# Kernel optimization log

Hardware: AMD Instinct MI355X
Metric: run time of the kernel (lower is better)

## Reference

```python
import jax, jax.numpy as jnp
import numpy as np

N, E, DIM, H = 100000, 1600000, 128, 8
HD = DIM // H


def setup_inputs() -> dict:
    key = jax.random.key(0)
    ks = jax.random.split(key, 12)
    inp = {
        'x': jax.random.normal(ks[0], (N, DIM), dtype=jnp.float32),
        'src': jax.random.randint(ks[1], (E,), 0, N, dtype=jnp.int32),
        'dst': jax.random.randint(ks[2], (E,), 0, N, dtype=jnp.int32),
    }
    scale = 1.0 / np.sqrt(DIM)
    for i, nm in enumerate(['q', 'k', 'v', 'o']):
        inp['W' + nm] = jax.random.normal(ks[3 + 2 * i], (DIM, DIM), dtype=jnp.float32) * scale
        inp['b' + nm] = jax.random.normal(ks[4 + 2 * i], (DIM,), dtype=jnp.float32) * 0.01
    return inp


def reference(x, src, dst, Wq, bq, Wk, bk, Wv, bv, Wo, bo):
    n = x.shape[0]
    q = (x @ Wq + bq).reshape(n, H, HD)
    k = (x @ Wk + bk).reshape(n, H, HD)
    v = (x @ Wv + bv).reshape(n, H, HD)
    # per-edge score: dot(q[src], k[dst]) over head_dim  -> [E, H]
    scores = jnp.einsum('ehd,ehd->eh', q[src], k[dst]) / np.sqrt(HD).astype(np.float32)
    # edge softmax grouped by destination node
    m = jax.ops.segment_max(scores, dst, num_segments=n)        # [N, H]
    e = jnp.exp(scores - m[dst])                                 # [E, H]
    z = jax.ops.segment_sum(e, dst, num_segments=n)              # [N, H]
    attn = e / z[dst]                                            # [E, H]
    # weighted scatter-sum of source values into destinations
    agg = jax.ops.segment_sum(v[src] * attn[:, :, None], dst, num_segments=n)  # [N, H, HD]
    out = agg.reshape(n, DIM) @ Wo + bo
    return out
```

## Files before the change

### kernel.cpp

```cpp
#include <hip/hip_runtime.h>
#include <hip/hip_bf16.h>
#include <math.h>


#define CAP 64
#define CUR_STRIDE 16
#define BCHUNK 4096

typedef __attribute__((ext_vector_type(8))) short short8;
typedef __attribute__((ext_vector_type(4))) float f32x4;

__device__ inline unsigned short f2bf(float f) {
    unsigned u = __float_as_uint(f);
    unsigned r = u + 0x7fffu + ((u >> 16) & 1u);
    return (unsigned short)(r >> 16);
}
__device__ inline float bfhi2f(unsigned u) { return __uint_as_float(u & 0xffff0000u); }
__device__ inline float bflo2f(unsigned u) { return __uint_as_float(u << 16); }

__device__ inline float w_perm(const float* Wq, const float* Wk, const float* Wv,
                               int k, int c) {
    if (c < 256) {
        int g = c >> 2, r = c & 3;
        return (r < 2) ? Wq[k * 128 + 2 * g + r] : Wv[k * 128 + 2 * g + (r - 2)];
    }
    return Wk[k * 128 + (c - 256)];
}

__global__ void pack_b_kernel(const float* __restrict__ Wq, const float* __restrict__ Wk,
                              const float* __restrict__ Wv, const float* __restrict__ Wo,
                              const float* __restrict__ bq, const float* __restrict__ bk,
                              const float* __restrict__ bv,
                              short* __restrict__ BqkvP, short* __restrict__ BoP,
                              float* __restrict__ bqkv) {
    int t = blockIdx.x * 256 + threadIdx.x;
    if (t < 24 * 4 * 64 * 8) {
        int j = t & 7, l = (t >> 3) & 63, ks = (t >> 9) & 3, ct = t >> 11;
        int c = ct * 16 + (l & 15);
        int k = ks * 32 + (l >> 4) * 8 + j;
        BqkvP[t] = (short)f2bf(w_perm(Wq, Wk, Wv, k, c));
    }
    if (t < 8 * 4 * 64 * 8) {
        int j = t & 7, l = (t >> 3) & 63, ks = (t >> 9) & 3, ct = t >> 11;
        int c = ct * 16 + (l & 15);
        int k = ks * 32 + (l >> 4) * 8 + j;
        BoP[t] = (short)f2bf(Wo[k * 128 + c]);
    }
    if (t < 384) {
        float v;
        if (t < 256) {
            int g = t >> 2, r = t & 3;
            v = (r < 2) ? bq[2 * g + r] : bv[2 * g + (r - 2)];
        } else v = bk[t - 256];
        bqkv[t] = v;
    }
}

#define QKV_STRIDE 392
__global__ __launch_bounds__(256) void gemm_qkv_mfma(const float* __restrict__ A,
        const short* __restrict__ Bp, const float* __restrict__ bias,
        short* __restrict__ qv, short* __restrict__ kb, int M) {
    __shared__ short stage[4][16][QKV_STRIDE];
    int w = threadIdx.x >> 6, l = threadIdx.x & 63;
    int row0 = blockIdx.x * 64 + w * 16;
    int lr = l & 15, lk = l >> 4;

    f32x4 acc[24];
    #pragma unroll
    for (int ct = 0; ct < 24; ++ct) {
        float b = bias[ct * 16 + lr];
        acc[ct][0] = b; acc[ct][1] = b; acc[ct][2] = b; acc[ct][3] = b;
    }

    int arow = row0 + lr;
    bool rowok = arow < M;
    const float* arp = A + (size_t)arow * 128;

    #pragma unroll
    for (int ks = 0; ks < 4; ++ks) {
        f32x4 a0 = {0.f, 0.f, 0.f, 0.f}, a1 = {0.f, 0.f, 0.f, 0.f};
        if (rowok) {
            a0 = *(const f32x4*)(arp + ks * 32 + lk * 8);
            a1 = *(const f32x4*)(arp + ks * 32 + lk * 8 + 4);
        }
        short8 af;
        af[0] = (short)f2bf(a0[0]); af[1] = (short)f2bf(a0[1]);
        af[2] = (short)f2bf(a0[2]); af[3] = (short)f2bf(a0[3]);
        af[4] = (short)f2bf(a1[0]); af[5] = (short)f2bf(a1[1]);
        af[6] = (short)f2bf(a1[2]); af[7] = (short)f2bf(a1[3]);
        #pragma unroll
        for (int ct = 0; ct < 24; ++ct) {
            short8 bf = *(const short8*)(Bp + ((size_t)(ct * 4 + ks) * 64 + l) * 8);
            acc[ct] = __builtin_amdgcn_mfma_f32_16x16x32_bf16(af, bf, acc[ct], 0, 0, 0);
        }
    }

    #pragma unroll
    for (int ct = 0; ct < 24; ++ct) {
        int c = ct * 16 + lr;
        #pragma unroll
        for (int j = 0; j < 4; ++j)
            stage[w][lk * 4 + j][c] = (short)f2bf(acc[ct][j]);
    }
    __syncthreads();

    #pragma unroll
    for (int it = 0; it < 8; ++it) {
        int rr = it * 2 + (l >> 5);
        int row = row0 + rr;
        if (row < M) {
            short8 vqv = *(const short8*)&stage[w][rr][(l & 31) * 8];
            *(short8*)(qv + (size_t)row * 256 + (l & 31) * 8) = vqv;
        }
    }
    #pragma unroll
    for (int it = 0; it < 4; ++it) {
        int rr = it * 4 + (l >> 4);
        int row = row0 + rr;
        if (row < M) {
            short8 vk = *(const short8*)&stage[w][rr][256 + (l & 15) * 8];
            *(short8*)(kb + (size_t)row * 128 + (l & 15) * 8) = vk;
        }
    }
}

__global__ __launch_bounds__(256) void gemm_out_mfma(const short* __restrict__ A,
        const short* __restrict__ Bp, const float* __restrict__ bias,
        float* __restrict__ C, int M) {
    int w = threadIdx.x >> 6, l = threadIdx.x & 63;
    int row0 = blockIdx.x * 64 + w * 16;
    int lr = l & 15, lk = l >> 4;

    f32x4 acc[8];
    #pragma unroll
    for (int ct = 0; ct < 8; ++ct) {
        float b = bias[ct * 16 + lr];
        acc[ct][0] = b; acc[ct][1] = b; acc[ct][2] = b; acc[ct][3] = b;
    }

    int arow = row0 + lr;
    bool rowok = arow < M;
    const short* arp = A + (size_t)arow * 128;

    #pragma unroll
    for (int ks = 0; ks < 4; ++ks) {
        short8 af = {0, 0, 0, 0, 0, 0, 0, 0};
        if (rowok) af = *(const short8*)(arp + ks * 32 + lk * 8);
        #pragma unroll
        for (int ct = 0; ct < 8; ++ct) {
            short8 bf = *(const short8*)(Bp + ((size_t)(ct * 4 + ks) * 64 + l) * 8);
            acc[ct] = __builtin_amdgcn_mfma_f32_16x16x32_bf16(af, bf, acc[ct], 0, 0, 0);
        }
    }

    #pragma unroll
    for (int ct = 0; ct < 8; ++ct) {
        int c = ct * 16 + lr;
        #pragma unroll
        for (int j = 0; j < 4; ++j) {
            int r = row0 + lk * 4 + j;
            if (r < M) C[(size_t)r * 128 + c] = acc[ct][j];
        }
    }
}

__global__ __launch_bounds__(256) void build_kernel(const int* __restrict__ src,
        const int* __restrict__ dst, int* __restrict__ cursor, int* __restrict__ csr,
        int E, int per8) {
    int xcd = blockIdx.x & 7;
    int chunk = blockIdx.x >> 3;
    int lo = xcd * per8, hi = lo + per8;
    int base = chunk * BCHUNK;
    #pragma unroll
    for (int it = 0; it < BCHUNK / 256; ++it) {
        int e = base + it * 256 + threadIdx.x;
        if (e < E) {
            int d = dst[e];
            int s = src[e];
            if (d >= lo && d < hi) {
                int slot = atomicAdd(&cursor[d << 4], 1);
                if (slot < CAP) csr[((size_t)d << 6) + slot] = s;
            }
        }
    }
}

#define EDGE_BODY(ss)                                                          \
    {                                                                          \
        uint2 u = *(const uint2*)(qv + (size_t)(ss) * 256 + l * 4);            \
        float p = bflo2f(u.x) * kdx + bfhi2f(u.x) * kdy;                       \
        p += __shfl_xor(p, 1);                                                 \
        p += __shfl_xor(p, 2);                                                 \
        p += __shfl_xor(p, 4);                                                 \
        float e = __expf(p * 0.25f);                                           \
        z += e;                                                                \
        ax += e * bflo2f(u.y);                                                 \
        ay += e * bfhi2f(u.y);                                                 \
    }

__global__ __launch_bounds__(256) void edge_attn_fused(const short* __restrict__ qv,
        const short* __restrict__ kb, const int* __restrict__ cursor,
        const int* __restrict__ csr, short* __restrict__ agg, int N, int per8) {
    int wv = threadIdx.x >> 6;
    int l  = threadIdx.x & 63;
    int xcd = blockIdx.x & 7;
    int j   = blockIdx.x >> 3;
    int local = j * 4 + wv;
    if (local >= per8) return;
    int d = xcd * per8 + local;
    if (d >= N) return;

    int deg = cursor[d << 4];
    int n = (deg < CAP) ? deg : CAP;
    const int* ep = csr + ((size_t)d << 6);
    unsigned kpk = __builtin_nontemporal_load((const unsigned*)(kb + (size_t)d * 128 + 2 * l));
    float kdx = bflo2f(kpk), kdy = bfhi2f(kpk);

    float z = 0.f, ax = 0.f, ay = 0.f;
    int i = 0;
    for (; i + 4 <= n; i += 4) {
        int s0 = ep[i];
        int s1 = ep[i + 1];
        int s2 = ep[i + 2];
        int s3 = ep[i + 3];
        EDGE_BODY(s0)
        EDGE_BODY(s1)
        EDGE_BODY(s2)
        EDGE_BODY(s3)
    }
    for (; i < n; ++i) {
        int s0 = ep[i];
        EDGE_BODY(s0)
    }

    float zi = (z > 0.f) ? 1.0f / z : 0.f;
    unsigned pk = (unsigned)f2bf(ax * zi) | ((unsigned)f2bf(ay * zi) << 16);
    *(unsigned*)(agg + (size_t)d * 128 + 2 * l) = pk;
}

extern "C" void kernel_launch(void* const* d_in, const int* in_sizes, int n_in,
                              void* d_out, int out_size, void* d_ws, size_t ws_size,
                              hipStream_t stream) {
    const float* x   = (const float*)d_in[0];
    const int*   src = (const int*)d_in[1];
    const int*   dst = (const int*)d_in[2];
    const float* Wq  = (const float*)d_in[3];
    const float* bq  = (const float*)d_in[4];
    const float* Wk  = (const float*)d_in[5];
    const float* bk  = (const float*)d_in[6];
    const float* Wv  = (const float*)d_in[7];
    const float* bv  = (const float*)d_in[8];
    const float* Wo  = (const float*)d_in[9];
    const float* bo  = (const float*)d_in[10];
    float* out = (float*)d_out;

    int N = in_sizes[0] / 128;
    int E = in_sizes[1];
    int per8 = (N + 7) / 8;

    char* ws = (char*)d_ws;
    size_t off = 0;
    auto alloc = [&](size_t bytes) -> void* {
        void* p = ws + off;
        off = (off + bytes + 255) & ~(size_t)255;
        return p;
    };
    short* BqkvP  = (short*)alloc((size_t)24 * 4 * 64 * 8 * 2);
    short* BoP    = (short*)alloc((size_t)8 * 4 * 64 * 8 * 2);
    float* bqkv   = (float*)alloc(384 * 4);
    short* qv     = (short*)alloc((size_t)N * 256 * 2);
    short* kb     = (short*)alloc((size_t)N * 128 * 2);
    short* agg    = (short*)alloc((size_t)N * 128 * 2);
    int* csr      = (int*)alloc((size_t)N * CAP * 4);
    int* cursor   = (int*)alloc((size_t)N * CUR_STRIDE * 4);
    (void)ws_size; (void)n_in; (void)out_size;

    hipMemsetAsync(cursor, 0, (size_t)N * CUR_STRIDE * 4, stream);

    pack_b_kernel<<<192, 256, 0, stream>>>(Wq, Wk, Wv, Wo, bq, bk, bv, BqkvP, BoP, bqkv);

    gemm_qkv_mfma<<<(N + 63) / 64, 256, 0, stream>>>(x, BqkvP, bqkv, qv, kb, N);

    int nchunks = (E + BCHUNK - 1) / BCHUNK;
    build_kernel<<<nchunks * 8, 256, 0, stream>>>(src, dst, cursor, csr, E, per8);

    int bpx = (per8 + 3) / 4;
    edge_attn_fused<<<bpx * 8, 256, 0, stream>>>(qv, kb, cursor, csr, agg, N, per8);

    gemm_out_mfma<<<(N + 63) / 64, 256, 0, stream>>>(agg, BoP, bo, out, N);
}
```

Baseline: 287.8 us.

## Fuse CSR build into QKV GEMM launch and output GEMM into edge kernel

```diff
diff --git a/kernel.cpp b/kernel.cpp
--- a/kernel.cpp
+++ b/kernel.cpp
@@ -57,12 +57,36 @@
 }
 
 #define QKV_STRIDE 392
-__global__ __launch_bounds__(256) void gemm_qkv_mfma(const float* __restrict__ A,
+__global__ __launch_bounds__(256) void qkv_build_kernel(const float* __restrict__ A,
         const short* __restrict__ Bp, const float* __restrict__ bias,
-        short* __restrict__ qv, short* __restrict__ kb, int M) {
+        short* __restrict__ qv, short* __restrict__ kb, int M,
+        const int* __restrict__ src, const int* __restrict__ dst,
+        int* __restrict__ cursor, int* __restrict__ csr, int E, int per8, int nBuild) {
     __shared__ short stage[4][16][QKV_STRIDE];
+    int bid = blockIdx.x;
+
+    if (bid < nBuild) {
+        int xcd = bid & 7;
+        int chunk = bid >> 3;
+        int lo = xcd * per8, hi = lo + per8;
+        int base = chunk * BCHUNK;
+        #pragma unroll
+        for (int it = 0; it < BCHUNK / 256; ++it) {
+            int e = base + it * 256 + threadIdx.x;
+            if (e < E) {
+                int d = dst[e];
+                int s = src[e];
+                if (d >= lo && d < hi) {
+                    int slot = atomicAdd(&cursor[d << 4], 1);
+                    if (slot < CAP) csr[((size_t)d << 6) + slot] = s;
+                }
+            }
+        }
+        return;
+    }
+
     int w = threadIdx.x >> 6, l = threadIdx.x & 63;
-    int row0 = blockIdx.x * 64 + w * 16;
+    int row0 = (bid - nBuild) * 64 + w * 16;
     int lr = l & 15, lk = l >> 4;
 
     f32x4 acc[24];
@@ -120,67 +144,6 @@
         if (row < M) {
             short8 vk = *(const short8*)&stage[w][rr][256 + (l & 15) * 8];
             *(short8*)(kb + (size_t)row * 128 + (l & 15) * 8) = vk;
-        }
-    }
-}
-
-__global__ __launch_bounds__(256) void gemm_out_mfma(const short* __restrict__ A,
-        const short* __restrict__ Bp, const float* __restrict__ bias,
-        float* __restrict__ C, int M) {
-    int w = threadIdx.x >> 6, l = threadIdx.x & 63;
-    int row0 = blockIdx.x * 64 + w * 16;
-    int lr = l & 15, lk = l >> 4;
-
-    f32x4 acc[8];
-    #pragma unroll
-    for (int ct = 0; ct < 8; ++ct) {
-        float b = bias[ct * 16 + lr];
-        acc[ct][0] = b; acc[ct][1] = b; acc[ct][2] = b; acc[ct][3] = b;
-    }
-
-    int arow = row0 + lr;
-    bool rowok = arow < M;
-    const short* arp = A + (size_t)arow * 128;
-
-    #pragma unroll
-    for (int ks = 0; ks < 4; ++ks) {
-        short8 af = {0, 0, 0, 0, 0, 0, 0, 0};
-        if (rowok) af = *(const short8*)(arp + ks * 32 + lk * 8);
-        #pragma unroll
-        for (int ct = 0; ct < 8; ++ct) {
-            short8 bf = *(const short8*)(Bp + ((size_t)(ct * 4 + ks) * 64 + l) * 8);
-            acc[ct] = __builtin_amdgcn_mfma_f32_16x16x32_bf16(af, bf, acc[ct], 0, 0, 0);
-        }
-    }
-
-    #pragma unroll
-    for (int ct = 0; ct < 8; ++ct) {
-        int c = ct * 16 + lr;
-        #pragma unroll
-        for (int j = 0; j < 4; ++j) {
-            int r = row0 + lk * 4 + j;
-            if (r < M) C[(size_t)r * 128 + c] = acc[ct][j];
-        }
-    }
-}
-
-__global__ __launch_bounds__(256) void build_kernel(const int* __restrict__ src,
-        const int* __restrict__ dst, int* __restrict__ cursor, int* __restrict__ csr,
-        int E, int per8) {
-    int xcd = blockIdx.x & 7;
-    int chunk = blockIdx.x >> 3;
-    int lo = xcd * per8, hi = lo + per8;
-    int base = chunk * BCHUNK;
-    #pragma unroll
-    for (int it = 0; it < BCHUNK / 256; ++it) {
-        int e = base + it * 256 + threadIdx.x;
-        if (e < E) {
-            int d = dst[e];
-            int s = src[e];
-            if (d >= lo && d < hi) {
-                int slot = atomicAdd(&cursor[d << 4], 1);
-                if (slot < CAP) csr[((size_t)d << 6) + slot] = s;
-            }
         }
     }
 }
@@ -198,44 +161,84 @@
         ay += e * bfhi2f(u.y);                                                 \
     }
 
-__global__ __launch_bounds__(256) void edge_attn_fused(const short* __restrict__ qv,
+#define AGG_STRIDE 68
+__global__ __launch_bounds__(256) void edge_out_kernel(const short* __restrict__ qv,
         const short* __restrict__ kb, const int* __restrict__ cursor,
-        const int* __restrict__ csr, short* __restrict__ agg, int N, int per8) {
-    int wv = threadIdx.x >> 6;
+        const int* __restrict__ csr, const short* __restrict__ BoP,
+        const float* __restrict__ bo, float* __restrict__ out, int N, int per8) {
+    __shared__ unsigned aggLds[4][16][AGG_STRIDE];
+    int w  = threadIdx.x >> 6;
     int l  = threadIdx.x & 63;
+    int lr = l & 15, lk = l >> 4;
     int xcd = blockIdx.x & 7;
-    int j   = blockIdx.x >> 3;
-    int local = j * 4 + wv;
-    if (local >= per8) return;
-    int d = xcd * per8 + local;
-    if (d >= N) return;
-
-    int deg = cursor[d << 4];
-    int n = (deg < CAP) ? deg : CAP;
-    const int* ep = csr + ((size_t)d << 6);
-    unsigned kpk = __builtin_nontemporal_load((const unsigned*)(kb + (size_t)d * 128 + 2 * l));
-    float kdx = bflo2f(kpk), kdy = bfhi2f(kpk);
-
-    float z = 0.f, ax = 0.f, ay = 0.f;
-    int i = 0;
-    for (; i + 4 <= n; i += 4) {
-        int s0 = ep[i];
-        int s1 = ep[i + 1];
-        int s2 = ep[i + 2];
-        int s3 = ep[i + 3];
-        EDGE_BODY(s0)
-        EDGE_BODY(s1)
-        EDGE_BODY(s2)
-        EDGE_BODY(s3)
-    }
-    for (; i < n; ++i) {
-        int s0 = ep[i];
-        EDGE_BODY(s0)
-    }
-
-    float zi = (z > 0.f) ? 1.0f / z : 0.f;
-    unsigned pk = (unsigned)f2bf(ax * zi) | ((unsigned)f2bf(ay * zi) << 16);
-    *(unsigned*)(agg + (size_t)d * 128 + 2 * l) = pk;
+    int jb  = blockIdx.x >> 3;
+    int sliceN = per8 < (N - xcd * per8) ? per8 : (N - xcd * per8);
+    int local0 = jb * 64 + w * 16;
+    int d0 = xcd * per8 + local0;
+
+    for (int i = 0; i < 16; ++i) {
+        int local = local0 + i;
+        if (local >= sliceN) break;
+        int d = xcd * per8 + local;
+
+        int deg = cursor[d << 4];
+        int n = (deg < CAP) ? deg : CAP;
+        const int* ep = csr + ((size_t)d << 6);
+        unsigned kpk = *(const unsigned*)(kb + (size_t)d * 128 + 2 * l);
+        float kdx = bflo2f(kpk), kdy = bfhi2f(kpk);
+
+        float z = 0.f, ax = 0.f, ay = 0.f;
+        int ii = 0;
+        for (; ii + 4 <= n; ii += 4) {
+            int s0 = ep[ii];
+            int s1 = ep[ii + 1];
+            int s2 = ep[ii + 2];
+            int s3 = ep[ii + 3];
+            EDGE_BODY(s0)
+            EDGE_BODY(s1)
+            EDGE_BODY(s2)
+            EDGE_BODY(s3)
+        }
+        for (; ii < n; ++ii) {
+            int s0 = ep[ii];
+            EDGE_BODY(s0)
+        }
+
+        float zi = (z > 0.f) ? 1.0f / z : 0.f;
+        unsigned pk = (unsigned)f2bf(ax * zi) | ((unsigned)f2bf(ay * zi) << 16);
+        aggLds[w][i][l] = pk;
+    }
+
+    f32x4 acc[8];
+    #pragma unroll
+    for (int ct = 0; ct < 8; ++ct) {
+        float b = bo[ct * 16 + lr];
+        acc[ct][0] = b; acc[ct][1] = b; acc[ct][2] = b; acc[ct][3] = b;
+    }
+
+    #pragma unroll
+    for (int ks = 0; ks < 4; ++ks) {
+        short8 af = *(const short8*)&aggLds[w][lr][ks * 16 + lk * 4];
+        #pragma unroll
+        for (int ct = 0; ct < 8; ++ct) {
+            short8 bf = *(const short8*)(BoP + ((size_t)(ct * 4 + ks) * 64 + l) * 8);
+            acc[ct] = __builtin_amdgcn_mfma_f32_16x16x32_bf16(af, bf, acc[ct], 0, 0, 0);
+        }
+    }
+
+    #pragma unroll
+    for (int ct = 0; ct < 8; ++ct) {
+        int c = ct * 16 + lr;
+        #pragma unroll
+        for (int j = 0; j < 4; ++j) {
+            int localr = local0 + lk * 4 + j;
+            if (localr < sliceN) {
+                int r = xcd * per8 + localr;
+                out[(size_t)r * 128 + c] = acc[ct][j];
+            }
+        }
+    }
+    (void)d0;
 }
 
 extern "C" void kernel_launch(void* const* d_in, const int* in_sizes, int n_in,
@@ -270,7 +273,6 @@
     float* bqkv   = (float*)alloc(384 * 4);
     short* qv     = (short*)alloc((size_t)N * 256 * 2);
     short* kb     = (short*)alloc((size_t)N * 128 * 2);
-    short* agg    = (short*)alloc((size_t)N * 128 * 2);
     int* csr      = (int*)alloc((size_t)N * CAP * 4);
     int* cursor   = (int*)alloc((size_t)N * CUR_STRIDE * 4);
     (void)ws_size; (void)n_in; (void)out_size;
@@ -279,13 +281,11 @@
 
     pack_b_kernel<<<192, 256, 0, stream>>>(Wq, Wk, Wv, Wo, bq, bk, bv, BqkvP, BoP, bqkv);
 
-    gemm_qkv_mfma<<<(N + 63) / 64, 256, 0, stream>>>(x, BqkvP, bqkv, qv, kb, N);
-
-    int nchunks = (E + BCHUNK - 1) / BCHUNK;
-    build_kernel<<<nchunks * 8, 256, 0, stream>>>(src, dst, cursor, csr, E, per8);
-
-    int bpx = (per8 + 3) / 4;
-    edge_attn_fused<<<bpx * 8, 256, 0, stream>>>(qv, kb, cursor, csr, agg, N, per8);
-
-    gemm_out_mfma<<<(N + 63) / 64, 256, 0, stream>>>(agg, BoP, bo, out, N);
-}
+    int nBuild = ((E + BCHUNK - 1) / BCHUNK) * 8;
+    int nGemm  = (N + 63) / 64;
+    qkv_build_kernel<<<nBuild + nGemm, 256, 0, stream>>>(x, BqkvP, bqkv, qv, kb, N,
+                                                         src, dst, cursor, csr, E, per8, nBuild);
+
+    int nb8 = (per8 + 63) / 64;
+    edge_out_kernel<<<nb8 * 8, 256, 0, stream>>>(qv, kb, cursor, csr, BoP, bo, out, N, per8);
+}
```

Measured after the change: 352.4 us. 1.22x slower.
